# Kernel optimization log

Measured on AMD Instinct MI355X. Metric: run time of the kernel, lower is better.

The kernel has to match this reference:

```python
import jax, jax.numpy as jnp
import numpy as np
import math

D_MODEL = 1024
N_HEADS = 16
B, S = 4, 2048

def _xavier(key, shape):
    fan_out, fan_in = shape
    limit = math.sqrt(6.0 / (fan_in + fan_out))
    return jax.random.uniform(key, shape, jnp.float32, -limit, limit)

def setup_inputs() -> dict:
    key = jax.random.key(0)
    kx, kqkv, ko = jax.random.split(key, 3)
    x = jax.random.normal(kx, (B, S, D_MODEL), dtype=jnp.float32)
    W_qkv = _xavier(kqkv, (3 * D_MODEL, D_MODEL))
    W_o = _xavier(ko, (D_MODEL, D_MODEL))
    return {"x": x, "W_qkv": W_qkv, "W_o": W_o}

def reference(x, W_qkv, W_o):
    Bx, Sx, D = x.shape
    H = N_HEADS
    d_h = D // H
    T = jnp.einsum('bsd,ed->bse', x, W_qkv)          # (B,S,3D)
    Q, K, V = jnp.split(T, 3, axis=-1)
    # (B,S,D) -> (B,H,S,d_h)
    Q = Q.reshape(Bx, Sx, H, d_h).transpose(0, 2, 1, 3)
    K = K.reshape(Bx, Sx, H, d_h).transpose(0, 2, 1, 3)
    V = V.reshape(Bx, Sx, H, d_h).transpose(0, 2, 1, 3)
    scores = jnp.einsum('bhqd,bhkd->bhqk', Q, K) / jnp.sqrt(jnp.float32(d_h))
    attn = jax.nn.softmax(scores, axis=-1)
    out = jnp.einsum('bhqk,bhkd->bhqd', attn, V)
    out = out.transpose(0, 2, 1, 3).reshape(Bx, Sx, D)
    Y = jnp.einsum('bsd,ed->bse', out, W_o)
    return Y
```

## Files before the change

### kernel.cpp

```cpp
#include <hip/hip_runtime.h>
#include <stdint.h>

#define SS 2048

typedef __attribute__((ext_vector_type(8))) short short8;
typedef __attribute__((ext_vector_type(4))) float f32x4;
typedef __attribute__((ext_vector_type(16))) float f32x16;

static __device__ __forceinline__ unsigned short f2bf(float f) {
    uint32_t u = __builtin_bit_cast(uint32_t, f);
    u += 0x7fffu + ((u >> 16) & 1u);
    return (unsigned short)(u >> 16);
}

static __device__ __forceinline__ uint32_t cvtpk(float lo, float hi) {
    uint32_t r;
    asm("v_cvt_pk_bf16_f32 %0, %1, %2" : "=v"(r) : "v"(lo), "v"(hi));
    return r;
}

static __device__ __forceinline__ void async16(const unsigned short* g, unsigned short* l) {
    __builtin_amdgcn_global_load_lds(
        (const __attribute__((address_space(1))) uint32_t*)g,
        (__attribute__((address_space(3))) uint32_t*)l, 16, 0, 0);
}

__global__ void cast3(const float* __restrict__ a, const float* __restrict__ b,
                      const float* __restrict__ c,
                      unsigned short* __restrict__ da, unsigned short* __restrict__ db,
                      unsigned short* __restrict__ dc_) {
    int i = (blockIdx.x * 256 + threadIdx.x) * 4;
    const float* s;
    unsigned short* d;
    if (i < 8388608)        { s = a + i;              d = da + i; }
    else if (i < 11534336)  { s = b + (i - 8388608);  d = db + (i - 8388608); }
    else                    { s = c + (i - 11534336); d = dc_ + (i - 11534336); }
    float4 v = *(const float4*)s;
    ushort4 o;
    o.x = f2bf(v.x); o.y = f2bf(v.y); o.z = f2bf(v.z); o.w = f2bf(v.w);
    *(ushort4*)d = o;
}

template<int MODE>
__global__ void gemm_bt(const unsigned short* __restrict__ A,
                        const unsigned short* __restrict__ Bm,
                        void* __restrict__ Cout,
                        unsigned short* __restrict__ Vt,
                        int K) {
    __shared__ unsigned short As[128 * 64];
    __shared__ unsigned short Bs[128 * 64];
    const int t = threadIdx.x;
    const int w = t >> 6, l = t & 63;
    const int wm = w >> 1, wn = w & 1;
    const int l15 = l & 15, l4 = l >> 4;
    const int m0 = blockIdx.x * 128, n0 = blockIdx.y * 128;
    const int srow = t >> 3;
    const int scol = (t & 7) * 8;

    f32x4 acc[4][4] = {};

    for (int k0 = 0; k0 < K; k0 += 64) {
#pragma unroll
        for (int r = 0; r < 4; ++r) {
            int row = r * 32 + srow;
            async16(A + (size_t)(m0 + row) * K + k0 + scol, (unsigned short*)&As[row * 64 + scol]);
        }
#pragma unroll
        for (int r = 0; r < 4; ++r) {
            int row = r * 32 + srow;
            async16(Bm + (size_t)(n0 + row) * K + k0 + scol, (unsigned short*)&Bs[row * 64 + scol]);
        }
        __syncthreads();
#pragma unroll
        for (int kk = 0; kk < 64; kk += 32) {
            short8 af[4], bfr[4];
#pragma unroll
            for (int m = 0; m < 4; ++m)
                af[m] = *(const short8*)&As[(wm * 64 + m * 16 + l15) * 64 + kk + l4 * 8];
#pragma unroll
            for (int n = 0; n < 4; ++n)
                bfr[n] = *(const short8*)&Bs[(wn * 64 + n * 16 + l15) * 64 + kk + l4 * 8];
#pragma unroll
            for (int m = 0; m < 4; ++m)
#pragma unroll
                for (int n = 0; n < 4; ++n)
                    acc[m][n] = __builtin_amdgcn_mfma_f32_16x16x32_bf16(af[m], bfr[n], acc[m][n], 0, 0, 0);
        }
        __syncthreads();
    }

#pragma unroll
    for (int m = 0; m < 4; ++m) {
        int rbase = m0 + wm * 64 + m * 16 + l4 * 4;
#pragma unroll
        for (int n = 0; n < 4; ++n) {
            int c = n0 + wn * 64 + n * 16 + l15;
            f32x4 v = acc[m][n];
            if (MODE == 0) {
                if (c < 2048) {
                    float sc = (c < 1024) ? 0.18033688f : 1.0f;
                    unsigned short* T = (unsigned short*)Cout;
#pragma unroll
                    for (int r = 0; r < 4; ++r)
                        T[(size_t)(rbase + r) * 2048 + c] = f2bf(v[0 + r] * sc);
                } else {
                    int vv = c - 2048;
                    int hh = vv >> 6, d = vv & 63;
                    int bb = rbase >> 11, s = rbase & 2047;
                    ushort4 pk;
                    pk.x = f2bf(v[0]); pk.y = f2bf(v[1]); pk.z = f2bf(v[2]); pk.w = f2bf(v[3]);
                    *(ushort4*)&Vt[((size_t)(bb * 16 + hh) * 64 + d) * 2048 + s] = pk;
                }
            } else {
                float* C = (float*)Cout;
#pragma unroll
                for (int r = 0; r < 4; ++r)
                    C[(size_t)(rbase + r) * 1024 + c] = v[r];
            }
        }
    }
}

__global__ __launch_bounds__(256, 4) void attn_kernel(
        const unsigned short* __restrict__ Tqk,
        const unsigned short* __restrict__ Vt,
        unsigned short* __restrict__ Out) {
    __shared__ unsigned short Ks[2][64 * 64];
    __shared__ unsigned short Vs[2][64 * 64];
    const int t = threadIdx.x;
    const int w = t >> 6, l = t & 63;
    const int lq = l & 31, hfl = l >> 5;

    const int lin = blockIdx.x;
    const int j = lin >> 3;
    const int bh = (lin & 7) * 8 + (j & 7);
    const int qt = j >> 3;
    const int b = bh >> 4, hh = bh & 15;
    const int qrow = qt * 128 + w * 32 + lq;

    short8 qf[4];
    const size_t trow = ((size_t)b * SS + qrow) * 2048;
#pragma unroll
    for (int dc = 0; dc < 4; ++dc)
        qf[dc] = *(const short8*)&Tqk[trow + hh * 64 + dc * 16 + hfl * 8];

    char* KsB = (char*)Ks;
    char* VsB = (char*)Vs;

    const int srow = t >> 3;
    const int scb = (t & 7) << 4;
    const int ssw = scb ^ ((srow & 7) << 4);
    const int sel = scb >> 1;

    const unsigned short* kp0 = Tqk + (size_t)b * SS * 2048 + 1024 + hh * 64 + (size_t)srow * 2048 + sel;
    const unsigned short* kp1 = kp0 + 32 * 2048;
    const unsigned short* vp0 = Vt + (size_t)bh * 64 * 2048 + (size_t)srow * 2048 + sel;
    const unsigned short* vp1 = vp0 + 32 * 2048;

    int4 kr0, kr1, vr0, vr1;
#define ISSUE()                                                                      \
    kr0 = *(const int4*)kp0; kr1 = *(const int4*)kp1;                                \
    vr0 = *(const int4*)vp0; vr1 = *(const int4*)vp1;
#define WRITE(buf)                                                                   \
    {                                                                                \
        char* kb = KsB + (buf) * 8192;                                               \
        char* vb = VsB + (buf) * 8192;                                               \
        *(int4*)(kb + srow * 128 + ssw) = kr0;                                       \
        *(int4*)(kb + (srow + 32) * 128 + ssw) = kr1;                                \
        *(int4*)(vb + srow * 128 + ssw) = vr0;                                       \
        *(int4*)(vb + (srow + 32) * 128 + ssw) = vr1;                                \
    }

    f32x16 oacc[2] = {};
    float la0 = 0.f, la1 = 0.f, la2 = 0.f, la3 = 0.f;

    ISSUE();
    WRITE(0);
    __syncthreads();

    for (int it = 0; it < 32; ++it) {
        const int cur = it & 1;
        const char* kb = KsB + cur * 8192;
        const char* vb = VsB + cur * 8192;
        const bool more = (it < 31);
        if (more) {
            kp0 += 64 * 2048; kp1 += 64 * 2048;
            vp0 += 64;        vp1 += 64;
            ISSUE();
        }

        f32x16 sa[2] = {};
        __builtin_amdgcn_s_setprio(1);
#pragma unroll
        for (int kvt = 0; kvt < 2; ++kvt) {
            int row = kvt * 32 + lq;
#pragma unroll
            for (int dc = 0; dc < 4; ++dc) {
                short8 kf = *(const short8*)(kb + row * 128 + ((dc * 32 + hfl * 16) ^ ((row & 7) << 4)));
                sa[kvt] = __builtin_amdgcn_mfma_f32_32x32x16_bf16(kf, qf[dc], sa[kvt], 0, 0, 0);
            }
        }
        __builtin_amdgcn_s_setprio(0);

#pragma unroll
        for (int kvt = 0; kvt < 2; ++kvt)
#pragma unroll
            for (int r = 0; r < 16; r += 4) {
                float p0 = __builtin_amdgcn_exp2f(sa[kvt][r + 0]);
                float p1 = __builtin_amdgcn_exp2f(sa[kvt][r + 1]);
                float p2 = __builtin_amdgcn_exp2f(sa[kvt][r + 2]);
                float p3 = __builtin_amdgcn_exp2f(sa[kvt][r + 3]);
                sa[kvt][r + 0] = p0; la0 += p0;
                sa[kvt][r + 1] = p1; la1 += p1;
                sa[kvt][r + 2] = p2; la2 += p2;
                sa[kvt][r + 3] = p3; la3 += p3;
            }

        short8 pb[4];
#pragma unroll
        for (int c = 0; c < 4; ++c) {
            int f = c >> 1, r0 = (c & 1) * 8;
            uint32_t v0 = cvtpk(sa[f][r0 + 0], sa[f][r0 + 1]);
            uint32_t v1 = cvtpk(sa[f][r0 + 2], sa[f][r0 + 3]);
            uint32_t v2 = cvtpk(sa[f][r0 + 4], sa[f][r0 + 5]);
            uint32_t v3 = cvtpk(sa[f][r0 + 6], sa[f][r0 + 7]);
            asm("v_permlane32_swap_b32 %0, %1" : "+v"(v0), "+v"(v2));
            asm("v_permlane32_swap_b32 %0, %1" : "+v"(v1), "+v"(v3));
            union { uint32_t u[4]; short8 s; } pbu;
            pbu.u[0] = v0;
            pbu.u[1] = v1;
            pbu.u[2] = v2;
            pbu.u[3] = v3;
            pb[c] = pbu.s;
        }

        __builtin_amdgcn_s_setprio(1);
#pragma unroll
        for (int dt = 0; dt < 2; ++dt) {
            int row0 = dt * 32 + lq;
#pragma unroll
            for (int c = 0; c < 4; ++c) {
                short8 vf = *(const short8*)(vb + row0 * 128 + ((c * 32 + hfl * 16) ^ ((row0 & 7) << 4)));
                oacc[dt] = __builtin_amdgcn_mfma_f32_32x32x16_bf16(vf, pb[c], oacc[dt], 0, 0, 0);
            }
        }
        __builtin_amdgcn_s_setprio(0);

        if (more) { WRITE(cur ^ 1); }
        __syncthreads();
    }
#undef ISSUE
#undef WRITE

    float l_run = (la0 + la1) + (la2 + la3);
    l_run += __shfl_xor(l_run, 32);
    float inv = 1.0f / l_run;
    const size_t obase = ((size_t)b * SS + qrow) * 1024 + hh * 64;
#pragma unroll
    for (int dt = 0; dt < 2; ++dt)
#pragma unroll
        for (int g = 0; g < 4; ++g) {
            int d0 = dt * 32 + 8 * g + 4 * hfl;
            ushort4 pk;
            pk.x = f2bf(oacc[dt][4 * g + 0] * inv);
            pk.y = f2bf(oacc[dt][4 * g + 1] * inv);
            pk.z = f2bf(oacc[dt][4 * g + 2] * inv);
            pk.w = f2bf(oacc[dt][4 * g + 3] * inv);
            *(ushort4*)&Out[obase + d0] = pk;
        }
}

extern "C" void kernel_launch(void* const* d_in, const int* in_sizes, int n_in,
                              void* d_out, int out_size, void* d_ws, size_t ws_size,
                              hipStream_t stream) {
    const float* x    = (const float*)d_in[0];
    const float* wqkv = (const float*)d_in[1];
    const float* wo   = (const float*)d_in[2];

    unsigned short* ws  = (unsigned short*)d_ws;
    unsigned short* xb  = ws;
    unsigned short* w1  = ws + 8388608;
    unsigned short* w2  = ws + 11534336;
    unsigned short* vt  = ws + 12582912;
    unsigned short* ao  = ws + 20971520;
    unsigned short* tqk = (unsigned short*)d_out;

    cast3<<<12288, 256, 0, stream>>>(x, wqkv, wo, xb, w1, w2);
    gemm_bt<0><<<dim3(64, 24), 256, 0, stream>>>(xb, w1, (void*)tqk, vt, 1024);
    attn_kernel<<<1024, 256, 0, stream>>>(tqk, vt, ao);
    gemm_bt<1><<<dim3(64, 8), 256, 0, stream>>>(ao, w2, d_out, nullptr, 1024);
}
```

Measured before the change: 187.8 us.

## Replace QKV projection GEMM with pipelined 128x256 double-buffered swizzled kernel

Result: no change. 190.2 us (+1.3%).

```diff
diff --git a/kernel.cpp b/kernel.cpp
--- a/kernel.cpp
+++ b/kernel.cpp
@@ -41,12 +41,123 @@
     *(ushort4*)d = o;
 }
 
-template<int MODE>
+__global__ __launch_bounds__(512, 1) void gemm0_qkv(
+        const unsigned short* __restrict__ A,
+        const unsigned short* __restrict__ B,
+        unsigned short* __restrict__ Tqk,
+        unsigned short* __restrict__ Vt) {
+    extern __shared__ char sm[];
+    const int t = threadIdx.x, w = t >> 6, l = t & 63;
+    const int wm = w >> 2, wn = w & 3;
+    const int l15 = l & 15, l4 = l >> 4;
+    const int lr = l >> 3, lc = l & 7;
+
+    const int lin = blockIdx.x;
+    const int wg = (lin & 7) * 96 + (lin >> 3);
+    const int bm = wg & 63, bn = wg >> 6;
+    const int m0 = bm * 128, n0 = bn * 256;
+
+    const int u_a = wn;
+    const int u_b = wm * 2 + (wn & 1);
+    const int scol = (lc ^ lr) * 8;
+
+    const unsigned short* Ab = A + (size_t)(m0 + wm * 64 + u_a * 8 + lr) * 1024 + scol;
+    const unsigned short* Bb = B + (size_t)(n0 + (wn >> 1) * 128 + u_b * 8 + lr) * 1024 + scol;
+
+    char* const smA = sm + wm * 8192;
+    char* const smB = sm + 32768 + (wn >> 1) * 16384;
+    const int adst = (u_a * 8 + lr) * 128 + lc * 16;
+    const int bdst = (u_b * 8 + lr) * 128 + lc * 16;
+
+#define SA(j, T, buf) async16(Ab + (size_t)(j) * 32768 + (size_t)(T) * 64, \
+        (unsigned short*)(smA + (buf) * 16384 + (j) * 4096 + adst))
+#define SB(j, T, buf) async16(Bb + (size_t)((((j) & 1) * 64 + ((j) >> 1) * 32)) * 1024 + (size_t)(T) * 64, \
+        (unsigned short*)(smB + (buf) * 32768 + ((((j) & 1) * 64 + ((j) >> 1) * 32)) * 128 + bdst))
+
+    const int rc0 = (l4 ^ (l15 & 7)) * 16;
+    const int rc1 = ((4 + l4) ^ (l15 & 7)) * 16;
+    const int brow = ((wn & 1) * 64 + l15) * 128;
+
+    f32x4 acc[4][4] = {};
+    short8 af[2][2], bfr[2][2];
+
+#define RD_A(lo) { const char* Ar = smA + cur * 16384 + (lo) * 4096 + l15 * 128;     \
+    af[0][0] = *(const short8*)(Ar + rc0);                                           \
+    af[0][1] = *(const short8*)(Ar + rc1);                                           \
+    af[1][0] = *(const short8*)(Ar + 2048 + rc0);                                    \
+    af[1][1] = *(const short8*)(Ar + 2048 + rc1); }
+#define RD_B(hi) { const char* Br = smB + cur * 32768 + brow + (hi) * 4096;          \
+    bfr[0][0] = *(const short8*)(Br + rc0);                                          \
+    bfr[0][1] = *(const short8*)(Br + rc1);                                          \
+    bfr[1][0] = *(const short8*)(Br + 2048 + rc0);                                   \
+    bfr[1][1] = *(const short8*)(Br + 2048 + rc1); }
+#define MM(R, C) _Pragma("unroll") for (int m = 0; m < 2; ++m)                       \
+    _Pragma("unroll") for (int n = 0; n < 2; ++n) {                                  \
+        acc[(R)*2+m][(C)*2+n] = __builtin_amdgcn_mfma_f32_16x16x32_bf16(             \
+            af[m][0], bfr[n][0], acc[(R)*2+m][(C)*2+n], 0, 0, 0);                    \
+        acc[(R)*2+m][(C)*2+n] = __builtin_amdgcn_mfma_f32_16x16x32_bf16(             \
+            af[m][1], bfr[n][1], acc[(R)*2+m][(C)*2+n], 0, 0, 0); }
+#define BAR __builtin_amdgcn_s_barrier()
+#define SP1 __builtin_amdgcn_s_setprio(1)
+#define SP0 __builtin_amdgcn_s_setprio(0)
+
+    SA(0, 0, 0); SB(0, 0, 0); SB(1, 0, 0); SA(1, 0, 0); SB(2, 0, 0); SB(3, 0, 0);
+
+    for (int tt = 0; tt < 16; ++tt) {
+        const int cur = tt & 1, nxt = cur ^ 1;
+        const int Tn = (tt + 1 < 16) ? tt + 1 : 0;
+        asm volatile("s_waitcnt vmcnt(3)" ::: "memory"); BAR;
+        RD_A(0); RD_B(0);
+        SA(0, Tn, nxt); SB(0, Tn, nxt);
+        SP1; MM(0, 0); SP0; BAR;
+        asm volatile("s_waitcnt vmcnt(4)" ::: "memory"); BAR;
+        RD_A(1);
+        SB(1, Tn, nxt); SA(1, Tn, nxt);
+        SP1; MM(1, 0); SP0; BAR;
+        asm volatile("s_waitcnt vmcnt(4)" ::: "memory"); BAR;
+        RD_B(1);
+        SB(2, Tn, nxt);
+        SP1; MM(1, 1); SP0; BAR;
+        RD_A(0);
+        SB(3, Tn, nxt);
+        SP1; MM(0, 1); SP0; BAR;
+    }
+#undef SA
+#undef SB
+#undef RD_A
+#undef RD_B
+#undef MM
+#undef BAR
+#undef SP1
+#undef SP0
+
+#pragma unroll
+    for (int fm = 0; fm < 4; ++fm) {
+        int rbase = m0 + wm * 64 + fm * 16 + l4 * 4;
+#pragma unroll
+        for (int fn = 0; fn < 4; ++fn) {
+            int c = n0 + wn * 64 + fn * 16 + l15;
+            f32x4 v = acc[fm][fn];
+            if (c < 2048) {
+                float sc = (c < 1024) ? 0.18033688f : 1.0f;
+#pragma unroll
+                for (int r = 0; r < 4; ++r)
+                    Tqk[(size_t)(rbase + r) * 2048 + c] = f2bf(v[r] * sc);
+            } else {
+                int vv = c - 2048;
+                int hh = vv >> 6, d = vv & 63;
+                int bb = rbase >> 11, s = rbase & 2047;
+                ushort4 pk;
+                pk.x = f2bf(v[0]); pk.y = f2bf(v[1]); pk.z = f2bf(v[2]); pk.w = f2bf(v[3]);
+                *(ushort4*)&Vt[((size_t)(bb * 16 + hh) * 64 + d) * 2048 + s] = pk;
+            }
+        }
+    }
+}
+
 __global__ void gemm_bt(const unsigned short* __restrict__ A,
                         const unsigned short* __restrict__ Bm,
-                        void* __restrict__ Cout,
-                        unsigned short* __restrict__ Vt,
-                        int K) {
+                        float* __restrict__ C, int K) {
     __shared__ unsigned short As[128 * 64];
     __shared__ unsigned short Bs[128 * 64];
     const int t = threadIdx.x;
@@ -96,27 +207,9 @@
         for (int n = 0; n < 4; ++n) {
             int c = n0 + wn * 64 + n * 16 + l15;
             f32x4 v = acc[m][n];
-            if (MODE == 0) {
-                if (c < 2048) {
-                    float sc = (c < 1024) ? 0.18033688f : 1.0f;
-                    unsigned short* T = (unsigned short*)Cout;
-#pragma unroll
-                    for (int r = 0; r < 4; ++r)
-                        T[(size_t)(rbase + r) * 2048 + c] = f2bf(v[0 + r] * sc);
-                } else {
-                    int vv = c - 2048;
-                    int hh = vv >> 6, d = vv & 63;
-                    int bb = rbase >> 11, s = rbase & 2047;
-                    ushort4 pk;
-                    pk.x = f2bf(v[0]); pk.y = f2bf(v[1]); pk.z = f2bf(v[2]); pk.w = f2bf(v[3]);
-                    *(ushort4*)&Vt[((size_t)(bb * 16 + hh) * 64 + d) * 2048 + s] = pk;
-                }
-            } else {
-                float* C = (float*)Cout;
-#pragma unroll
-                for (int r = 0; r < 4; ++r)
-                    C[(size_t)(rbase + r) * 1024 + c] = v[r];
-            }
+#pragma unroll
+            for (int r = 0; r < 4; ++r)
+                C[(size_t)(rbase + r) * 1024 + c] = v[r];
         }
     }
 }
@@ -285,8 +378,11 @@
     unsigned short* ao  = ws + 20971520;
     unsigned short* tqk = (unsigned short*)d_out;
 
+    (void)hipFuncSetAttribute((const void*)gemm0_qkv,
+                              hipFuncAttributeMaxDynamicSharedMemorySize, 98304);
+
     cast3<<<12288, 256, 0, stream>>>(x, wqkv, wo, xb, w1, w2);
-    gemm_bt<0><<<dim3(64, 24), 256, 0, stream>>>(xb, w1, (void*)tqk, vt, 1024);
+    gemm0_qkv<<<768, 512, 98304, stream>>>(xb, w1, tqk, vt);
     attn_kernel<<<1024, 256, 0, stream>>>(tqk, vt, ao);
-    gemm_bt<1><<<dim3(64, 8), 256, 0, stream>>>(ao, w2, d_out, nullptr, 1024);
-}
+    gemm_bt<<<dim3(64, 8), 256, 0, stream>>>(ao, w2, (float*)d_out, 1024);
+}
```

## Load K/V fragments directly from global memory, dropping LDS staging and barriers

Applied to the files above, without the earlier changes.

Result: slower. 333.0 us (+77.3%).

```diff
diff --git a/kernel.cpp b/kernel.cpp
--- a/kernel.cpp
+++ b/kernel.cpp
@@ -125,8 +125,6 @@
         const unsigned short* __restrict__ Tqk,
         const unsigned short* __restrict__ Vt,
         unsigned short* __restrict__ Out) {
-    __shared__ unsigned short Ks[2][64 * 64];
-    __shared__ unsigned short Vs[2][64 * 64];
     const int t = threadIdx.x;
     const int w = t >> 6, l = t & 63;
     const int lq = l & 31, hfl = l >> 5;
@@ -144,86 +142,53 @@
     for (int dc = 0; dc < 4; ++dc)
         qf[dc] = *(const short8*)&Tqk[trow + hh * 64 + dc * 16 + hfl * 8];
 
-    char* KsB = (char*)Ks;
-    char* VsB = (char*)Vs;
-
-    const int srow = t >> 3;
-    const int scb = (t & 7) << 4;
-    const int ssw = scb ^ ((srow & 7) << 4);
-    const int sel = scb >> 1;
-
-    const unsigned short* kp0 = Tqk + (size_t)b * SS * 2048 + 1024 + hh * 64 + (size_t)srow * 2048 + sel;
-    const unsigned short* kp1 = kp0 + 32 * 2048;
-    const unsigned short* vp0 = Vt + (size_t)bh * 64 * 2048 + (size_t)srow * 2048 + sel;
+    const unsigned short* kp  = Tqk + (size_t)b * SS * 2048 + 1024 + hh * 64
+                              + (size_t)lq * 2048 + hfl * 8;
+    const unsigned short* vp0 = Vt + (size_t)bh * 64 * 2048
+                              + (size_t)lq * 2048 + hfl * 8;
     const unsigned short* vp1 = vp0 + 32 * 2048;
-
-    int4 kr0, kr1, vr0, vr1;
-#define ISSUE()                                                                      \
-    kr0 = *(const int4*)kp0; kr1 = *(const int4*)kp1;                                \
-    vr0 = *(const int4*)vp0; vr1 = *(const int4*)vp1;
-#define WRITE(buf)                                                                   \
-    {                                                                                \
-        char* kb = KsB + (buf) * 8192;                                               \
-        char* vb = VsB + (buf) * 8192;                                               \
-        *(int4*)(kb + srow * 128 + ssw) = kr0;                                       \
-        *(int4*)(kb + (srow + 32) * 128 + ssw) = kr1;                                \
-        *(int4*)(vb + srow * 128 + ssw) = vr0;                                       \
-        *(int4*)(vb + (srow + 32) * 128 + ssw) = vr1;                                \
-    }
 
     f32x16 oacc[2] = {};
     float la0 = 0.f, la1 = 0.f, la2 = 0.f, la3 = 0.f;
 
-    ISSUE();
-    WRITE(0);
-    __syncthreads();
-
-    for (int it = 0; it < 32; ++it) {
-        const int cur = it & 1;
-        const char* kb = KsB + cur * 8192;
-        const char* vb = VsB + cur * 8192;
-        const bool more = (it < 31);
-        if (more) {
-            kp0 += 64 * 2048; kp1 += 64 * 2048;
-            vp0 += 64;        vp1 += 64;
-            ISSUE();
-        }
-
-        f32x16 sa[2] = {};
+    for (int it = 0; it < 64; ++it) {
+        short8 kf0 = *(const short8*)(kp);
+        short8 kf1 = *(const short8*)(kp + 16);
+        short8 kf2 = *(const short8*)(kp + 32);
+        short8 kf3 = *(const short8*)(kp + 48);
+        short8 vf00 = *(const short8*)(vp0);
+        short8 vf01 = *(const short8*)(vp0 + 16);
+        short8 vf10 = *(const short8*)(vp1);
+        short8 vf11 = *(const short8*)(vp1 + 16);
+
+        f32x16 sa = {};
         __builtin_amdgcn_s_setprio(1);
-#pragma unroll
-        for (int kvt = 0; kvt < 2; ++kvt) {
-            int row = kvt * 32 + lq;
-#pragma unroll
-            for (int dc = 0; dc < 4; ++dc) {
-                short8 kf = *(const short8*)(kb + row * 128 + ((dc * 32 + hfl * 16) ^ ((row & 7) << 4)));
-                sa[kvt] = __builtin_amdgcn_mfma_f32_32x32x16_bf16(kf, qf[dc], sa[kvt], 0, 0, 0);
-            }
-        }
+        sa = __builtin_amdgcn_mfma_f32_32x32x16_bf16(kf0, qf[0], sa, 0, 0, 0);
+        sa = __builtin_amdgcn_mfma_f32_32x32x16_bf16(kf1, qf[1], sa, 0, 0, 0);
+        sa = __builtin_amdgcn_mfma_f32_32x32x16_bf16(kf2, qf[2], sa, 0, 0, 0);
+        sa = __builtin_amdgcn_mfma_f32_32x32x16_bf16(kf3, qf[3], sa, 0, 0, 0);
         __builtin_amdgcn_s_setprio(0);
 
 #pragma unroll
-        for (int kvt = 0; kvt < 2; ++kvt)
-#pragma unroll
-            for (int r = 0; r < 16; r += 4) {
-                float p0 = __builtin_amdgcn_exp2f(sa[kvt][r + 0]);
-                float p1 = __builtin_amdgcn_exp2f(sa[kvt][r + 1]);
-                float p2 = __builtin_amdgcn_exp2f(sa[kvt][r + 2]);
-                float p3 = __builtin_amdgcn_exp2f(sa[kvt][r + 3]);
-                sa[kvt][r + 0] = p0; la0 += p0;
-                sa[kvt][r + 1] = p1; la1 += p1;
-                sa[kvt][r + 2] = p2; la2 += p2;
-                sa[kvt][r + 3] = p3; la3 += p3;
-            }
-
-        short8 pb[4];
-#pragma unroll
-        for (int c = 0; c < 4; ++c) {
-            int f = c >> 1, r0 = (c & 1) * 8;
-            uint32_t v0 = cvtpk(sa[f][r0 + 0], sa[f][r0 + 1]);
-            uint32_t v1 = cvtpk(sa[f][r0 + 2], sa[f][r0 + 3]);
-            uint32_t v2 = cvtpk(sa[f][r0 + 4], sa[f][r0 + 5]);
-            uint32_t v3 = cvtpk(sa[f][r0 + 6], sa[f][r0 + 7]);
+        for (int r = 0; r < 16; r += 4) {
+            float p0 = __builtin_amdgcn_exp2f(sa[r + 0]);
+            float p1 = __builtin_amdgcn_exp2f(sa[r + 1]);
+            float p2 = __builtin_amdgcn_exp2f(sa[r + 2]);
+            float p3 = __builtin_amdgcn_exp2f(sa[r + 3]);
+            sa[r + 0] = p0; la0 += p0;
+            sa[r + 1] = p1; la1 += p1;
+            sa[r + 2] = p2; la2 += p2;
+            sa[r + 3] = p3; la3 += p3;
+        }
+
+        short8 pb[2];
+#pragma unroll
+        for (int c = 0; c < 2; ++c) {
+            int r0 = c * 8;
+            uint32_t v0 = cvtpk(sa[r0 + 0], sa[r0 + 1]);
+            uint32_t v1 = cvtpk(sa[r0 + 2], sa[r0 + 3]);
+            uint32_t v2 = cvtpk(sa[r0 + 4], sa[r0 + 5]);
+            uint32_t v3 = cvtpk(sa[r0 + 6], sa[r0 + 7]);
             asm("v_permlane32_swap_b32 %0, %1" : "+v"(v0), "+v"(v2));
             asm("v_permlane32_swap_b32 %0, %1" : "+v"(v1), "+v"(v3));
             union { uint32_t u[4]; short8 s; } pbu;
@@ -235,22 +200,16 @@
         }
 
         __builtin_amdgcn_s_setprio(1);
-#pragma unroll
-        for (int dt = 0; dt < 2; ++dt) {
-            int row0 = dt * 32 + lq;
-#pragma unroll
-            for (int c = 0; c < 4; ++c) {
-                short8 vf = *(const short8*)(vb + row0 * 128 + ((c * 32 + hfl * 16) ^ ((row0 & 7) << 4)));
-                oacc[dt] = __builtin_amdgcn_mfma_f32_32x32x16_bf16(vf, pb[c], oacc[dt], 0, 0, 0);
-            }
-        }
+        oacc[0] = __builtin_amdgcn_mfma_f32_32x32x16_bf16(vf00, pb[0], oacc[0], 0, 0, 0);
+        oacc[0] = __builtin_amdgcn_mfma_f32_32x32x16_bf16(vf01, pb[1], oacc[0], 0, 0, 0);
+        oacc[1] = __builtin_amdgcn_mfma_f32_32x32x16_bf16(vf10, pb[0], oacc[1], 0, 0, 0);
+        oacc[1] = __builtin_amdgcn_mfma_f32_32x32x16_bf16(vf11, pb[1], oacc[1], 0, 0, 0);
         __builtin_amdgcn_s_setprio(0);
 
-        if (more) { WRITE(cur ^ 1); }
-        __syncthreads();
+        kp  += 32 * 2048;
+        vp0 += 32;
+        vp1 += 32;
     }
-#undef ISSUE
-#undef WRITE
 
     float l_run = (la0 + la1) + (la2 + la3);
     l_run += __shfl_xor(l_run, 32);
```
